# Optimization experiments

Hardware: AMD Instinct MI355X
Metric: run time of the kernel (lower is better)

The kernel has to match this reference:

```python
import jax, jax.numpy as jnp
import numpy as np
from jax import lax

Z_SIZE = 512
M = 512
HH = 511
BATCH = 65536


def setup_inputs() -> dict:
    key = jax.random.key(0)
    ks = jax.random.split(key, 5)
    z = jax.random.normal(ks[0], (BATCH, Z_SIZE), dtype=jnp.float32)
    # params initialized uniform(-1, 1) as in init_params
    v = jax.random.uniform(ks[1], (HH, Z_SIZE), dtype=jnp.float32, minval=-1.0, maxval=1.0)
    Rs = jax.random.uniform(ks[2], (M, M), dtype=jnp.float32, minval=-1.0, maxval=1.0)
    r2diag = jax.random.uniform(ks[3], (M,), dtype=jnp.float32, minval=-1.0, maxval=1.0)
    c = jax.random.uniform(ks[4], (1, M), dtype=jnp.float32, minval=-1.0, maxval=1.0)
    return {"z": z, "v": v, "Rs": Rs, "r2diag": r2diag, "c": c}


def _create_q(v):
    # normalize each Householder vector
    vn = v / jnp.linalg.norm(v, axis=1, keepdims=True)  # (hh, z)
    # q = prod_i (I - 2 v_i v_i^T), applied left-to-right.
    # Rank-1 update form: q <- q - 2 (q v_i) v_i^T  (O(n^2) per step).
    def body(q, vi):
        q = q - 2.0 * jnp.outer(q @ vi, vi)
        return q, None
    q, _ = lax.scan(body, jnp.eye(Z_SIZE, dtype=v.dtype), vn)
    return q[:, :M]  # (z_size, m)


def _create_rs(Rs, r2diag):
    r1 = jnp.triu(Rs, k=0)                     # (m, m)
    r2 = jnp.triu(Rs, k=1) + jnp.diag(r2diag)  # strict upper + learned diagonal
    return r1, r2


def reference(z, v, Rs, r2diag, c):
    r1, r2 = _create_rs(Rs, r2diag)
    q = _create_q(v)                 # (z, m)
    Bt = q @ r2.T                    # (z, m)
    A = q @ r1                       # (z, m)
    Btzc = z @ Bt + c                # (B, m)
    hB = jnp.tanh(Btzc)
    z_out = hB @ A.T + z             # (B, z)
    rrii = jnp.diagonal(r1) * jnp.diagonal(r2)  # (m,)
    der = 1.0 - hB * hB              # tanh'
    ldj = jnp.sum(jnp.log(jnp.abs(der * rrii + 1.0)), axis=1)  # (B,)
    return z_out, ldj
```

## Files before the change

kernel.cpp:

```cpp
#include <hip/hip_runtime.h>
#include <math.h>
#include <stdint.h>

#define ZDIM   512
#define MDIM   512
#define HHN    511
#define NBATCH 65536

typedef float f32x4 __attribute__((ext_vector_type(4)));
typedef short s16x8 __attribute__((ext_vector_type(8)));

__device__ __forceinline__ uint32_t bf16rne(float x) {
    uint32_t u = __float_as_uint(x);
    return (u + 0x7fffu + ((u >> 16) & 1u)) >> 16;
}
__device__ __forceinline__ void split2(float x, short& h, short& l) {
    uint32_t hu = bf16rne(x);
    float hf = __uint_as_float(hu << 16);
    uint32_t lu = bf16rne(x - hf);
    h = (short)hu; l = (short)lu;
}

__global__ void __launch_bounds__(64) prep_kernel(const float* __restrict__ v,
                                                  const float* __restrict__ Rs,
                                                  const float* __restrict__ r2diag,
                                                  float* __restrict__ vn,
                                                  float* __restrict__ rrii) {
    int b    = blockIdx.x;
    int lane = threadIdx.x;
    if (b < HHN) {
        const float4* src = reinterpret_cast<const float4*>(v + (size_t)b * ZDIM);
        float4 a0 = src[lane * 2];
        float4 a1 = src[lane * 2 + 1];
        float s = a0.x*a0.x + a0.y*a0.y + a0.z*a0.z + a0.w*a0.w
                + a1.x*a1.x + a1.y*a1.y + a1.z*a1.z + a1.w*a1.w;
#pragma unroll
        for (int off = 32; off >= 1; off >>= 1) s += __shfl_xor(s, off, 64);
        float inv = 1.0f / sqrtf(s);
        float4 o0 = make_float4(a0.x*inv, a0.y*inv, a0.z*inv, a0.w*inv);
        float4 o1 = make_float4(a1.x*inv, a1.y*inv, a1.z*inv, a1.w*inv);
        float4* dst = reinterpret_cast<float4*>(vn + (size_t)b * ZDIM);
        dst[lane * 2]     = o0;
        dst[lane * 2 + 1] = o1;
    } else {
        for (int m = lane; m < MDIM; m += 64)
            rrii[m] = Rs[(size_t)m * MDIM + m] * r2diag[m];
    }
}

__global__ void __launch_bounds__(256) householder_kernel(const float* __restrict__ vn,
                                                          float* __restrict__ Q) {
    int wave = threadIdx.x >> 6;
    int lane = threadIdx.x & 63;
    int r    = blockIdx.x * 4 + wave;

    float q[8];
#pragma unroll
    for (int j = 0; j < 8; ++j) q[j] = 0.0f;
    int base = r - lane * 8;
    if (base >= 0 && base < 8) q[base] = 1.0f;

    const float4* vn4 = reinterpret_cast<const float4*>(vn);
    float4 va = vn4[lane * 2];
    float4 vb = vn4[lane * 2 + 1];
    for (int i = 0; i < HHN; ++i) {
        float4 ca = va, cb = vb;
        if (i + 1 < HHN) {
            va = vn4[(size_t)(i + 1) * (ZDIM / 4) + lane * 2];
            vb = vn4[(size_t)(i + 1) * (ZDIM / 4) + lane * 2 + 1];
        }
        float d = q[0]*ca.x + q[1]*ca.y + q[2]*ca.z + q[3]*ca.w
                + q[4]*cb.x + q[5]*cb.y + q[6]*cb.z + q[7]*cb.w;
#pragma unroll
        for (int off = 32; off >= 1; off >>= 1) d += __shfl_xor(d, off, 64);
        float s = -2.0f * d;
        q[0] = fmaf(s, ca.x, q[0]); q[1] = fmaf(s, ca.y, q[1]);
        q[2] = fmaf(s, ca.z, q[2]); q[3] = fmaf(s, ca.w, q[3]);
        q[4] = fmaf(s, cb.x, q[4]); q[5] = fmaf(s, cb.y, q[5]);
        q[6] = fmaf(s, cb.z, q[6]); q[7] = fmaf(s, cb.w, q[7]);
    }
    float4* qdst = reinterpret_cast<float4*>(Q + (size_t)r * ZDIM);
    qdst[lane * 2]     = make_float4(q[0], q[1], q[2], q[3]);
    qdst[lane * 2 + 1] = make_float4(q[4], q[5], q[6], q[7]);
}

__global__ void __launch_bounds__(256) small_gemm_kernel(const float* __restrict__ Q,
                                                         const float* __restrict__ Rs,
                                                         const float* __restrict__ r2diag,
                                                         short* __restrict__ Ah_g,
                                                         short* __restrict__ Al_g,
                                                         short* __restrict__ B1h_g,
                                                         short* __restrict__ B1l_g) {
    int r0 = blockIdx.y * 64;
    int c0 = blockIdx.x * 64;
    int tid = threadIdx.x;
    int tx = tid & 15, ty = tid >> 4;

    __shared__ float Qs[16][68];
    __shared__ float RA[16][68];
    __shared__ float RB[16][68];

    float accA[4][4] = {};
    float accB[4][4] = {};

    for (int k0 = 0; k0 < ZDIM; k0 += 16) {
        {
            int r = tid >> 2, c4 = tid & 3;
            float4 g = *reinterpret_cast<const float4*>(Q + (size_t)(r0 + r) * ZDIM + k0 + c4 * 4);
            Qs[c4*4+0][r] = g.x; Qs[c4*4+1][r] = g.y; Qs[c4*4+2][r] = g.z; Qs[c4*4+3][r] = g.w;
        }
        {
            int kk = tid >> 4, c4 = tid & 15;
            int kg = k0 + kk, cg = c0 + c4 * 4;
            float4 g = *reinterpret_cast<const float4*>(Rs + (size_t)kg * MDIM + cg);
            float4 m;
            m.x = (kg <= cg + 0) ? g.x : 0.0f;
            m.y = (kg <= cg + 1) ? g.y : 0.0f;
            m.z = (kg <= cg + 2) ? g.z : 0.0f;
            m.w = (kg <= cg + 3) ? g.w : 0.0f;
            *reinterpret_cast<float4*>(&RA[kk][c4 * 4]) = m;
        }
        {
            int c = tid >> 2, k4 = tid & 3;
            int cg = c0 + c;
            float4 g = *reinterpret_cast<const float4*>(Rs + (size_t)cg * MDIM + k0 + k4 * 4);
            float gv[4] = {g.x, g.y, g.z, g.w};
#pragma unroll
            for (int qq = 0; qq < 4; ++qq) {
                int kg = k0 + k4 * 4 + qq;
                float val = (kg > cg) ? gv[qq] : ((kg == cg) ? r2diag[cg] : 0.0f);
                RB[k4 * 4 + qq][c] = val;
            }
        }
        __syncthreads();
#pragma unroll
        for (int kk = 0; kk < 16; ++kk) {
            float4 aq = *reinterpret_cast<const float4*>(&Qs[kk][ty * 4]);
            float4 ra = *reinterpret_cast<const float4*>(&RA[kk][tx * 4]);
            float4 rb = *reinterpret_cast<const float4*>(&RB[kk][tx * 4]);
            float av[4]  = {aq.x, aq.y, aq.z, aq.w};
            float rav[4] = {ra.x, ra.y, ra.z, ra.w};
            float rbv[4] = {rb.x, rb.y, rb.z, rb.w};
#pragma unroll
            for (int i = 0; i < 4; ++i)
#pragma unroll
                for (int j = 0; j < 4; ++j) {
                    accA[i][j] = fmaf(av[i], rav[j], accA[i][j]);
                    accB[i][j] = fmaf(av[i], rbv[j], accB[i][j]);
                }
        }
        __syncthreads();
    }
#pragma unroll
    for (int i = 0; i < 4; ++i) {
        int rg = r0 + ty * 4 + i;
#pragma unroll
        for (int j = 0; j < 4; ++j) {
            int cg = c0 + tx * 4 + j;
            short h, l;
            split2(accA[i][j], h, l);
            Ah_g[(size_t)rg * MDIM + cg] = h;
            Al_g[(size_t)rg * MDIM + cg] = l;
            split2(accB[i][j], h, l);
            B1h_g[(size_t)cg * ZDIM + rg] = h;
            B1l_g[(size_t)cg * ZDIM + rg] = l;
        }
    }
}

__global__ void __launch_bounds__(256, 2) gemm1_mfma(const float* __restrict__ z,
                                                     const short* __restrict__ B1h,
                                                     const short* __restrict__ B1l,
                                                     const float* __restrict__ cvec,
                                                     const float* __restrict__ rrii,
                                                     uint32_t* __restrict__ hBp,
                                                     float* __restrict__ ldj) {
    int b0 = blockIdx.x * 128;
    int c0 = blockIdx.y * 256;
    int tid = threadIdx.x;

    __shared__ short Azh[128][40], Azl[128][40];
    __shared__ short Bsh[256][40], Bsl[256][40];

    int wid = tid >> 6, lane = tid & 63;
    int wm = wid >> 1, wn = wid & 1;
    int lrow = lane & 15, lk = (lane >> 4) * 8;

    f32x4 acc[4][8];
#pragma unroll
    for (int m = 0; m < 4; ++m)
#pragma unroll
        for (int n = 0; n < 8; ++n) acc[m][n] = (f32x4){0.f, 0.f, 0.f, 0.f};

    for (int k0 = 0; k0 < ZDIM; k0 += 32) {
        {
            int r = tid >> 1, half = tid & 1;
            const float* zp = z + (size_t)(b0 + r) * ZDIM + k0 + half * 16;
            float xv[16];
            *reinterpret_cast<float4*>(&xv[0])  = *reinterpret_cast<const float4*>(zp);
            *reinterpret_cast<float4*>(&xv[4])  = *reinterpret_cast<const float4*>(zp + 4);
            *reinterpret_cast<float4*>(&xv[8])  = *reinterpret_cast<const float4*>(zp + 8);
            *reinterpret_cast<float4*>(&xv[12]) = *reinterpret_cast<const float4*>(zp + 12);
            s16x8 h0, h1, l0, l1;
#pragma unroll
            for (int j = 0; j < 8; ++j) { short hh, ll; split2(xv[j],     hh, ll); h0[j] = hh; l0[j] = ll; }
#pragma unroll
            for (int j = 0; j < 8; ++j) { short hh, ll; split2(xv[8 + j], hh, ll); h1[j] = hh; l1[j] = ll; }
            *reinterpret_cast<s16x8*>(&Azh[r][half * 16])     = h0;
            *reinterpret_cast<s16x8*>(&Azh[r][half * 16 + 8]) = h1;
            *reinterpret_cast<s16x8*>(&Azl[r][half * 16])     = l0;
            *reinterpret_cast<s16x8*>(&Azl[r][half * 16 + 8]) = l1;
        }
        {
            const short* ph = B1h + (size_t)(c0 + tid) * ZDIM + k0;
            const short* pl = B1l + (size_t)(c0 + tid) * ZDIM + k0;
#pragma unroll
            for (int s = 0; s < 4; ++s)
                *reinterpret_cast<s16x8*>(&Bsh[tid][s * 8]) = *reinterpret_cast<const s16x8*>(ph + s * 8);
#pragma unroll
            for (int s = 0; s < 4; ++s)
                *reinterpret_cast<s16x8*>(&Bsl[tid][s * 8]) = *reinterpret_cast<const s16x8*>(pl + s * 8);
        }
        __syncthreads();

        s16x8 ah[4], al[4];
#pragma unroll
        for (int m = 0; m < 4; ++m) {
            ah[m] = *reinterpret_cast<const s16x8*>(&Azh[wm * 64 + m * 16 + lrow][lk]);
            al[m] = *reinterpret_cast<const s16x8*>(&Azl[wm * 64 + m * 16 + lrow][lk]);
        }
#pragma unroll
        for (int n = 0; n < 8; ++n) {
            s16x8 bh = *reinterpret_cast<const s16x8*>(&Bsh[wn * 128 + n * 16 + lrow][lk]);
            s16x8 bl = *reinterpret_cast<const s16x8*>(&Bsl[wn * 128 + n * 16 + lrow][lk]);
#pragma unroll
            for (int m = 0; m < 4; ++m) {
                acc[m][n] = __builtin_amdgcn_mfma_f32_16x16x32_bf16(ah[m], bh, acc[m][n], 0, 0, 0);
                acc[m][n] = __builtin_amdgcn_mfma_f32_16x16x32_bf16(al[m], bh, acc[m][n], 0, 0, 0);
                acc[m][n] = __builtin_amdgcn_mfma_f32_16x16x32_bf16(ah[m], bl, acc[m][n], 0, 0, 0);
            }
        }
        __syncthreads();
    }

    float cv[8], rr[8];
#pragma unroll
    for (int n = 0; n < 8; ++n) {
        int col = c0 + wn * 128 + n * 16 + lrow;
        cv[n] = cvec[col];
        rr[n] = rrii[col];
    }
    float lsum[4][4];
#pragma unroll
    for (int m = 0; m < 4; ++m)
#pragma unroll
        for (int r = 0; r < 4; ++r) lsum[m][r] = 0.0f;

#pragma unroll
    for (int m = 0; m < 4; ++m) {
#pragma unroll
        for (int r = 0; r < 4; ++r) {
            int b = b0 + wm * 64 + m * 16 + (lane >> 4) * 4 + r;
#pragma unroll
            for (int n = 0; n < 8; ++n) {
                float val = acc[m][n][r] + cv[n];
                float h = tanhf(val);
                short hh, ll;
                split2(h, hh, ll);
                int col = c0 + wn * 128 + n * 16 + lrow;
                hBp[(size_t)b * MDIM + col] = (uint32_t)(uint16_t)hh | ((uint32_t)(uint16_t)ll << 16);
                float der = 1.0f - h * h;
                lsum[m][r] += logf(fabsf(fmaf(der, rr[n], 1.0f)));
            }
        }
    }
#pragma unroll
    for (int m = 0; m < 4; ++m) {
#pragma unroll
        for (int r = 0; r < 4; ++r) {
            float s = lsum[m][r];
            s += __shfl_xor(s, 1, 64);
            s += __shfl_xor(s, 2, 64);
            s += __shfl_xor(s, 4, 64);
            s += __shfl_xor(s, 8, 64);
            if ((lane & 15) == 0)
                atomicAdd(&ldj[b0 + wm * 64 + m * 16 + (lane >> 4) * 4 + r], s);
        }
    }
}

__global__ void __launch_bounds__(512, 2) gemm2_mfma(const float* __restrict__ z,
                                                     const short* __restrict__ Ah_g,
                                                     const short* __restrict__ Al_g,
                                                     float* __restrict__ out) {
    int b0 = blockIdx.x * 128;
    int tid = threadIdx.x;
    const uint32_t* hBp = reinterpret_cast<const uint32_t*>(out);

    __shared__ short Hh[128][40], Hl[128][40];
    __shared__ short Ash[512][40], Asl[512][40];

    int wid = tid >> 6, lane = tid & 63;
    int wm = wid >> 2, wn = wid & 3;
    int lrow = lane & 15, lk = (lane >> 4) * 8;

    f32x4 acc[4][8];
#pragma unroll
    for (int m = 0; m < 4; ++m)
#pragma unroll
        for (int n = 0; n < 8; ++n) acc[m][n] = (f32x4){0.f, 0.f, 0.f, 0.f};

    for (int m0 = 0; m0 < MDIM; m0 += 32) {
        {
            int r = tid >> 2, q = tid & 3;
            const uint32_t* hp = hBp + (size_t)(b0 + r) * MDIM + m0 + q * 8;
            uint4 u0 = *reinterpret_cast<const uint4*>(hp);
            uint4 u1 = *reinterpret_cast<const uint4*>(hp + 4);
            uint32_t uv[8] = {u0.x, u0.y, u0.z, u0.w, u1.x, u1.y, u1.z, u1.w};
            s16x8 vh, vl;
#pragma unroll
            for (int j = 0; j < 8; ++j) {
                vh[j] = (short)(uv[j] & 0xffffu);
                vl[j] = (short)(uv[j] >> 16);
            }
            *reinterpret_cast<s16x8*>(&Hh[r][q * 8]) = vh;
            *reinterpret_cast<s16x8*>(&Hl[r][q * 8]) = vl;
        }
        {
            const short* ph = Ah_g + (size_t)tid * MDIM + m0;
            const short* pl = Al_g + (size_t)tid * MDIM + m0;
#pragma unroll
            for (int s = 0; s < 4; ++s)
                *reinterpret_cast<s16x8*>(&Ash[tid][s * 8]) = *reinterpret_cast<const s16x8*>(ph + s * 8);
#pragma unroll
            for (int s = 0; s < 4; ++s)
                *reinterpret_cast<s16x8*>(&Asl[tid][s * 8]) = *reinterpret_cast<const s16x8*>(pl + s * 8);
        }
        __syncthreads();

        s16x8 ah[4], al[4];
#pragma unroll
        for (int m = 0; m < 4; ++m) {
            ah[m] = *reinterpret_cast<const s16x8*>(&Hh[wm * 64 + m * 16 + lrow][lk]);
            al[m] = *reinterpret_cast<const s16x8*>(&Hl[wm * 64 + m * 16 + lrow][lk]);
        }
#pragma unroll
        for (int n = 0; n < 8; ++n) {
            s16x8 bh = *reinterpret_cast<const s16x8*>(&Ash[wn * 128 + n * 16 + lrow][lk]);
            s16x8 bl = *reinterpret_cast<const s16x8*>(&Asl[wn * 128 + n * 16 + lrow][lk]);
#pragma unroll
            for (int m = 0; m < 4; ++m) {
                acc[m][n] = __builtin_amdgcn_mfma_f32_16x16x32_bf16(ah[m], bh, acc[m][n], 0, 0, 0);
                acc[m][n] = __builtin_amdgcn_mfma_f32_16x16x32_bf16(al[m], bh, acc[m][n], 0, 0, 0);
                acc[m][n] = __builtin_amdgcn_mfma_f32_16x16x32_bf16(ah[m], bl, acc[m][n], 0, 0, 0);
            }
        }
        __syncthreads();
    }

#pragma unroll
    for (int m = 0; m < 4; ++m) {
#pragma unroll
        for (int r = 0; r < 4; ++r) {
            int b = b0 + wm * 64 + m * 16 + (lane >> 4) * 4 + r;
#pragma unroll
            for (int n = 0; n < 8; ++n) {
                int colz = wn * 128 + n * 16 + lrow;
                out[(size_t)b * ZDIM + colz] = acc[m][n][r] + z[(size_t)b * ZDIM + colz];
            }
        }
    }
}

extern "C" void kernel_launch(void* const* d_in, const int* in_sizes, int n_in,
                              void* d_out, int out_size, void* d_ws, size_t ws_size,
                              hipStream_t stream) {
    const float* z      = (const float*)d_in[0];
    const float* v      = (const float*)d_in[1];
    const float* Rs     = (const float*)d_in[2];
    const float* r2diag = (const float*)d_in[3];
    const float* cvec   = (const float*)d_in[4];

    float* out = (float*)d_out;
    float* ldj = out + (size_t)NBATCH * ZDIM;

    float* ws   = (float*)d_ws;
    float* vn   = ws;
    float* Q    = ws + 262144;
    float* rrii = ws + 524288;
    short* sbase = (short*)(ws + 524800);
    short* Ah_g = sbase;
    short* Al_g = sbase + 262144;
    short* B1h  = sbase + 2 * 262144;
    short* B1l  = sbase + 3 * 262144;

    hipMemsetAsync(ldj, 0, NBATCH * sizeof(float), stream);

    prep_kernel<<<512, 64, 0, stream>>>(v, Rs, r2diag, vn, rrii);
    householder_kernel<<<128, 256, 0, stream>>>(vn, Q);
    small_gemm_kernel<<<dim3(8, 8), 256, 0, stream>>>(Q, Rs, r2diag, Ah_g, Al_g, B1h, B1l);
    gemm1_mfma<<<dim3(512, 2), 256, 0, stream>>>(z, B1h, B1l, cvec, rrii,
                                                 (uint32_t*)out, ldj);
    gemm2_mfma<<<512, 512, 0, stream>>>(z, Ah_g, Al_g, out);
}
```

Measured before the change: 718.9 us.

## Double-buffer activation tiles, read weight fragments from global, batch Householder rows per wave

Both MFMA GEMMs now keep only the activation tile in double-buffered shared memory, prefetching the next k-slice while computing, and read the small weight fragments directly from global (L2-resident) with a one-step register prefetch instead of staging them through LDS. gemm1 now uses 512 threads covering all 512 output columns per block, so z is split once per row block rather than twice. The Householder kernel has each wave process four rows of Q at once, sharing the vn loads and interleaving the four shuffle reductions, with a quarter of the blocks. The cost is more registers per thread and uncoalesced global weight reads that rely on cache hits.

```diff
diff --git a/kernel.cpp b/kernel.cpp
--- a/kernel.cpp
+++ b/kernel.cpp
@@ -50,15 +50,21 @@
 
 __global__ void __launch_bounds__(256) householder_kernel(const float* __restrict__ vn,
                                                           float* __restrict__ Q) {
-    int wave = threadIdx.x >> 6;
+    int wid  = threadIdx.x >> 6;
     int lane = threadIdx.x & 63;
-    int r    = blockIdx.x * 4 + wave;
-
-    float q[8];
-#pragma unroll
-    for (int j = 0; j < 8; ++j) q[j] = 0.0f;
-    int base = r - lane * 8;
-    if (base >= 0 && base < 8) q[base] = 1.0f;
+    int wslot = blockIdx.x * 4 + wid;
+
+    float q[4][8];
+#pragma unroll
+    for (int c = 0; c < 4; ++c)
+#pragma unroll
+        for (int j = 0; j < 8; ++j) q[c][j] = 0.0f;
+#pragma unroll
+    for (int c = 0; c < 4; ++c) {
+        int r = wslot * 4 + c;
+        int base = r - lane * 8;
+        if (base >= 0 && base < 8) q[c][base] = 1.0f;
+    }
 
     const float4* vn4 = reinterpret_cast<const float4*>(vn);
     float4 va = vn4[lane * 2];
@@ -69,19 +75,32 @@
             va = vn4[(size_t)(i + 1) * (ZDIM / 4) + lane * 2];
             vb = vn4[(size_t)(i + 1) * (ZDIM / 4) + lane * 2 + 1];
         }
-        float d = q[0]*ca.x + q[1]*ca.y + q[2]*ca.z + q[3]*ca.w
-                + q[4]*cb.x + q[5]*cb.y + q[6]*cb.z + q[7]*cb.w;
-#pragma unroll
-        for (int off = 32; off >= 1; off >>= 1) d += __shfl_xor(d, off, 64);
-        float s = -2.0f * d;
-        q[0] = fmaf(s, ca.x, q[0]); q[1] = fmaf(s, ca.y, q[1]);
-        q[2] = fmaf(s, ca.z, q[2]); q[3] = fmaf(s, ca.w, q[3]);
-        q[4] = fmaf(s, cb.x, q[4]); q[5] = fmaf(s, cb.y, q[5]);
-        q[6] = fmaf(s, cb.z, q[6]); q[7] = fmaf(s, cb.w, q[7]);
-    }
-    float4* qdst = reinterpret_cast<float4*>(Q + (size_t)r * ZDIM);
-    qdst[lane * 2]     = make_float4(q[0], q[1], q[2], q[3]);
-    qdst[lane * 2 + 1] = make_float4(q[4], q[5], q[6], q[7]);
+        float d[4];
+#pragma unroll
+        for (int c = 0; c < 4; ++c)
+            d[c] = q[c][0]*ca.x + q[c][1]*ca.y + q[c][2]*ca.z + q[c][3]*ca.w
+                 + q[c][4]*cb.x + q[c][5]*cb.y + q[c][6]*cb.z + q[c][7]*cb.w;
+#pragma unroll
+        for (int off = 32; off >= 1; off >>= 1) {
+#pragma unroll
+            for (int c = 0; c < 4; ++c) d[c] += __shfl_xor(d[c], off, 64);
+        }
+#pragma unroll
+        for (int c = 0; c < 4; ++c) {
+            float s = -2.0f * d[c];
+            q[c][0] = fmaf(s, ca.x, q[c][0]); q[c][1] = fmaf(s, ca.y, q[c][1]);
+            q[c][2] = fmaf(s, ca.z, q[c][2]); q[c][3] = fmaf(s, ca.w, q[c][3]);
+            q[c][4] = fmaf(s, cb.x, q[c][4]); q[c][5] = fmaf(s, cb.y, q[c][5]);
+            q[c][6] = fmaf(s, cb.z, q[c][6]); q[c][7] = fmaf(s, cb.w, q[c][7]);
+        }
+    }
+#pragma unroll
+    for (int c = 0; c < 4; ++c) {
+        int r = wslot * 4 + c;
+        float4* qdst = reinterpret_cast<float4*>(Q + (size_t)r * ZDIM);
+        qdst[lane * 2]     = make_float4(q[c][0], q[c][1], q[c][2], q[c][3]);
+        qdst[lane * 2 + 1] = make_float4(q[c][4], q[c][5], q[c][6], q[c][7]);
+    }
 }
 
 __global__ void __launch_bounds__(256) small_gemm_kernel(const float* __restrict__ Q,
@@ -168,7 +187,7 @@
     }
 }
 
-__global__ void __launch_bounds__(256, 2) gemm1_mfma(const float* __restrict__ z,
+__global__ void __launch_bounds__(512, 2) gemm1_mfma(const float* __restrict__ z,
                                                      const short* __restrict__ B1h,
                                                      const short* __restrict__ B1l,
                                                      const float* __restrict__ cvec,
@@ -176,15 +195,14 @@
                                                      uint32_t* __restrict__ hBp,
                                                      float* __restrict__ ldj) {
     int b0 = blockIdx.x * 128;
-    int c0 = blockIdx.y * 256;
     int tid = threadIdx.x;
 
-    __shared__ short Azh[128][40], Azl[128][40];
-    __shared__ short Bsh[256][40], Bsl[256][40];
+    __shared__ short Azh[2][128][40], Azl[2][128][40];
 
     int wid = tid >> 6, lane = tid & 63;
-    int wm = wid >> 1, wn = wid & 1;
+    int wm = wid >> 2, wn = wid & 3;
     int lrow = lane & 15, lk = (lane >> 4) * 8;
+    int srow = tid >> 2, squar = tid & 3;
 
     f32x4 acc[4][8];
 #pragma unroll
@@ -192,53 +210,61 @@
 #pragma unroll
         for (int n = 0; n < 8; ++n) acc[m][n] = (f32x4){0.f, 0.f, 0.f, 0.f};
 
-    for (int k0 = 0; k0 < ZDIM; k0 += 32) {
-        {
-            int r = tid >> 1, half = tid & 1;
-            const float* zp = z + (size_t)(b0 + r) * ZDIM + k0 + half * 16;
-            float xv[16];
-            *reinterpret_cast<float4*>(&xv[0])  = *reinterpret_cast<const float4*>(zp);
-            *reinterpret_cast<float4*>(&xv[4])  = *reinterpret_cast<const float4*>(zp + 4);
-            *reinterpret_cast<float4*>(&xv[8])  = *reinterpret_cast<const float4*>(zp + 8);
-            *reinterpret_cast<float4*>(&xv[12]) = *reinterpret_cast<const float4*>(zp + 12);
-            s16x8 h0, h1, l0, l1;
-#pragma unroll
-            for (int j = 0; j < 8; ++j) { short hh, ll; split2(xv[j],     hh, ll); h0[j] = hh; l0[j] = ll; }
-#pragma unroll
-            for (int j = 0; j < 8; ++j) { short hh, ll; split2(xv[8 + j], hh, ll); h1[j] = hh; l1[j] = ll; }
-            *reinterpret_cast<s16x8*>(&Azh[r][half * 16])     = h0;
-            *reinterpret_cast<s16x8*>(&Azh[r][half * 16 + 8]) = h1;
-            *reinterpret_cast<s16x8*>(&Azl[r][half * 16])     = l0;
-            *reinterpret_cast<s16x8*>(&Azl[r][half * 16 + 8]) = l1;
-        }
-        {
-            const short* ph = B1h + (size_t)(c0 + tid) * ZDIM + k0;
-            const short* pl = B1l + (size_t)(c0 + tid) * ZDIM + k0;
-#pragma unroll
-            for (int s = 0; s < 4; ++s)
-                *reinterpret_cast<s16x8*>(&Bsh[tid][s * 8]) = *reinterpret_cast<const s16x8*>(ph + s * 8);
-#pragma unroll
-            for (int s = 0; s < 4; ++s)
-                *reinterpret_cast<s16x8*>(&Bsl[tid][s * 8]) = *reinterpret_cast<const s16x8*>(pl + s * 8);
-        }
-        __syncthreads();
-
+    float4 za, zb;
+    const float* zrow = z + (size_t)(b0 + srow) * ZDIM + squar * 8;
+    const short* bhbase = B1h + (size_t)(wn * 128 + lrow) * ZDIM + lk;
+    const short* blbase = B1l + (size_t)(wn * 128 + lrow) * ZDIM + lk;
+
+    za = *reinterpret_cast<const float4*>(zrow);
+    zb = *reinterpret_cast<const float4*>(zrow + 4);
+    {
+        s16x8 h, l;
+#pragma unroll
+        for (int j = 0; j < 4; ++j) { short hh, ll; split2((&za.x)[j], hh, ll); h[j] = hh; l[j] = ll; }
+#pragma unroll
+        for (int j = 0; j < 4; ++j) { short hh, ll; split2((&zb.x)[j], hh, ll); h[4+j] = hh; l[4+j] = ll; }
+        *reinterpret_cast<s16x8*>(&Azh[0][srow][squar * 8]) = h;
+        *reinterpret_cast<s16x8*>(&Azl[0][srow][squar * 8]) = l;
+    }
+    __syncthreads();
+
+    for (int t = 0; t < 16; ++t) {
+        int k0 = t * 32, cur = t & 1;
+        if (t + 1 < 16) {
+            za = *reinterpret_cast<const float4*>(zrow + (t + 1) * 32);
+            zb = *reinterpret_cast<const float4*>(zrow + (t + 1) * 32 + 4);
+        }
         s16x8 ah[4], al[4];
 #pragma unroll
         for (int m = 0; m < 4; ++m) {
-            ah[m] = *reinterpret_cast<const s16x8*>(&Azh[wm * 64 + m * 16 + lrow][lk]);
-            al[m] = *reinterpret_cast<const s16x8*>(&Azl[wm * 64 + m * 16 + lrow][lk]);
-        }
+            ah[m] = *reinterpret_cast<const s16x8*>(&Azh[cur][wm * 64 + m * 16 + lrow][lk]);
+            al[m] = *reinterpret_cast<const s16x8*>(&Azl[cur][wm * 64 + m * 16 + lrow][lk]);
+        }
+        s16x8 bh = *reinterpret_cast<const s16x8*>(bhbase + k0);
+        s16x8 bl = *reinterpret_cast<const s16x8*>(blbase + k0);
 #pragma unroll
         for (int n = 0; n < 8; ++n) {
-            s16x8 bh = *reinterpret_cast<const s16x8*>(&Bsh[wn * 128 + n * 16 + lrow][lk]);
-            s16x8 bl = *reinterpret_cast<const s16x8*>(&Bsl[wn * 128 + n * 16 + lrow][lk]);
+            s16x8 nbh, nbl;
+            if (n < 7) {
+                nbh = *reinterpret_cast<const s16x8*>(bhbase + (size_t)(n + 1) * 16 * ZDIM + k0);
+                nbl = *reinterpret_cast<const s16x8*>(blbase + (size_t)(n + 1) * 16 * ZDIM + k0);
+            }
 #pragma unroll
             for (int m = 0; m < 4; ++m) {
                 acc[m][n] = __builtin_amdgcn_mfma_f32_16x16x32_bf16(ah[m], bh, acc[m][n], 0, 0, 0);
                 acc[m][n] = __builtin_amdgcn_mfma_f32_16x16x32_bf16(al[m], bh, acc[m][n], 0, 0, 0);
                 acc[m][n] = __builtin_amdgcn_mfma_f32_16x16x32_bf16(ah[m], bl, acc[m][n], 0, 0, 0);
             }
+            bh = nbh; bl = nbl;
+        }
+        if (t + 1 < 16) {
+            s16x8 h, l;
+#pragma unroll
+            for (int j = 0; j < 4; ++j) { short hh, ll; split2((&za.x)[j], hh, ll); h[j] = hh; l[j] = ll; }
+#pragma unroll
+            for (int j = 0; j < 4; ++j) { short hh, ll; split2((&zb.x)[j], hh, ll); h[4+j] = hh; l[4+j] = ll; }
+            *reinterpret_cast<s16x8*>(&Azh[cur ^ 1][srow][squar * 8]) = h;
+            *reinterpret_cast<s16x8*>(&Azl[cur ^ 1][srow][squar * 8]) = l;
         }
         __syncthreads();
     }
@@ -246,7 +272,7 @@
     float cv[8], rr[8];
 #pragma unroll
     for (int n = 0; n < 8; ++n) {
-        int col = c0 + wn * 128 + n * 16 + lrow;
+        int col = wn * 128 + n * 16 + lrow;
         cv[n] = cvec[col];
         rr[n] = rrii[col];
     }
@@ -267,7 +293,7 @@
                 float h = tanhf(val);
                 short hh, ll;
                 split2(h, hh, ll);
-                int col = c0 + wn * 128 + n * 16 + lrow;
+                int col = wn * 128 + n * 16 + lrow;
                 hBp[(size_t)b * MDIM + col] = (uint32_t)(uint16_t)hh | ((uint32_t)(uint16_t)ll << 16);
                 float der = 1.0f - h * h;
                 lsum[m][r] += logf(fabsf(fmaf(der, rr[n], 1.0f)));
@@ -297,12 +323,12 @@
     int tid = threadIdx.x;
     const uint32_t* hBp = reinterpret_cast<const uint32_t*>(out);
 
-    __shared__ short Hh[128][40], Hl[128][40];
-    __shared__ short Ash[512][40], Asl[512][40];
+    __shared__ short Hh[2][128][40], Hl[2][128][40];
 
     int wid = tid >> 6, lane = tid & 63;
     int wm = wid >> 2, wn = wid & 3;
     int lrow = lane & 15, lk = (lane >> 4) * 8;
+    int srow = tid >> 2, squar = tid & 3;
 
     f32x4 acc[4][8];
 #pragma unroll
@@ -310,50 +336,59 @@
 #pragma unroll
         for (int n = 0; n < 8; ++n) acc[m][n] = (f32x4){0.f, 0.f, 0.f, 0.f};
 
-    for (int m0 = 0; m0 < MDIM; m0 += 32) {
-        {
-            int r = tid >> 2, q = tid & 3;
-            const uint32_t* hp = hBp + (size_t)(b0 + r) * MDIM + m0 + q * 8;
-            uint4 u0 = *reinterpret_cast<const uint4*>(hp);
-            uint4 u1 = *reinterpret_cast<const uint4*>(hp + 4);
-            uint32_t uv[8] = {u0.x, u0.y, u0.z, u0.w, u1.x, u1.y, u1.z, u1.w};
-            s16x8 vh, vl;
-#pragma unroll
-            for (int j = 0; j < 8; ++j) {
-                vh[j] = (short)(uv[j] & 0xffffu);
-                vl[j] = (short)(uv[j] >> 16);
-            }
-            *reinterpret_cast<s16x8*>(&Hh[r][q * 8]) = vh;
-            *reinterpret_cast<s16x8*>(&Hl[r][q * 8]) = vl;
-        }
-        {
-            const short* ph = Ah_g + (size_t)tid * MDIM + m0;
-            const short* pl = Al_g + (size_t)tid * MDIM + m0;
-#pragma unroll
-            for (int s = 0; s < 4; ++s)
-                *reinterpret_cast<s16x8*>(&Ash[tid][s * 8]) = *reinterpret_cast<const s16x8*>(ph + s * 8);
-#pragma unroll
-            for (int s = 0; s < 4; ++s)
-                *reinterpret_cast<s16x8*>(&Asl[tid][s * 8]) = *reinterpret_cast<const s16x8*>(pl + s * 8);
-        }
-        __syncthreads();
-
+    uint4 ua, ub;
+    const uint32_t* hrow = hBp + (size_t)(b0 + srow) * MDIM + squar * 8;
+    const short* bhbase = Ah_g + (size_t)(wn * 128 + lrow) * MDIM + lk;
+    const short* blbase = Al_g + (size_t)(wn * 128 + lrow) * MDIM + lk;
+
+    ua = *reinterpret_cast<const uint4*>(hrow);
+    ub = *reinterpret_cast<const uint4*>(hrow + 4);
+    {
+        s16x8 h, l;
+        uint32_t uv[8] = {ua.x, ua.y, ua.z, ua.w, ub.x, ub.y, ub.z, ub.w};
+#pragma unroll
+        for (int j = 0; j < 8; ++j) { h[j] = (short)(uv[j] & 0xffffu); l[j] = (short)(uv[j] >> 16); }
+        *reinterpret_cast<s16x8*>(&Hh[0][srow][squar * 8]) = h;
+        *reinterpret_cast<s16x8*>(&Hl[0][srow][squar * 8]) = l;
+    }
+    __syncthreads();
+
+    for (int t = 0; t < 16; ++t) {
+        int m0 = t * 32, cur = t & 1;
+        if (t + 1 < 16) {
+            ua = *reinterpret_cast<const uint4*>(hrow + (t + 1) * 32);
+            ub = *reinterpret_cast<const uint4*>(hrow + (t + 1) * 32 + 4);
+        }
         s16x8 ah[4], al[4];
 #pragma unroll
         for (int m = 0; m < 4; ++m) {
-            ah[m] = *reinterpret_cast<const s16x8*>(&Hh[wm * 64 + m * 16 + lrow][lk]);
-            al[m] = *reinterpret_cast<const s16x8*>(&Hl[wm * 64 + m * 16 + lrow][lk]);
-        }
+            ah[m] = *reinterpret_cast<const s16x8*>(&Hh[cur][wm * 64 + m * 16 + lrow][lk]);
+            al[m] = *reinterpret_cast<const s16x8*>(&Hl[cur][wm * 64 + m * 16 + lrow][lk]);
+        }
+        s16x8 bh = *reinterpret_cast<const s16x8*>(bhbase + m0);
+        s16x8 bl = *reinterpret_cast<const s16x8*>(blbase + m0);
 #pragma unroll
         for (int n = 0; n < 8; ++n) {
-            s16x8 bh = *reinterpret_cast<const s16x8*>(&Ash[wn * 128 + n * 16 + lrow][lk]);
-            s16x8 bl = *reinterpret_cast<const s16x8*>(&Asl[wn * 128 + n * 16 + lrow][lk]);
+            s16x8 nbh, nbl;
+            if (n < 7) {
+                nbh = *reinterpret_cast<const s16x8*>(bhbase + (size_t)(n + 1) * 16 * MDIM + m0);
+                nbl = *reinterpret_cast<const s16x8*>(blbase + (size_t)(n + 1) * 16 * MDIM + m0);
+            }
 #pragma unroll
             for (int m = 0; m < 4; ++m) {
                 acc[m][n] = __builtin_amdgcn_mfma_f32_16x16x32_bf16(ah[m], bh, acc[m][n], 0, 0, 0);
                 acc[m][n] = __builtin_amdgcn_mfma_f32_16x16x32_bf16(al[m], bh, acc[m][n], 0, 0, 0);
                 acc[m][n] = __builtin_amdgcn_mfma_f32_16x16x32_bf16(ah[m], bl, acc[m][n], 0, 0, 0);
             }
+            bh = nbh; bl = nbl;
+        }
+        if (t + 1 < 16) {
+            s16x8 h, l;
+            uint32_t uv[8] = {ua.x, ua.y, ua.z, ua.w, ub.x, ub.y, ub.z, ub.w};
+#pragma unroll
+            for (int j = 0; j < 8; ++j) { h[j] = (short)(uv[j] & 0xffffu); l[j] = (short)(uv[j] >> 16); }
+            *reinterpret_cast<s16x8*>(&Hh[cur ^ 1][srow][squar * 8]) = h;
+            *reinterpret_cast<s16x8*>(&Hl[cur ^ 1][srow][squar * 8]) = l;
         }
         __syncthreads();
     }
@@ -397,9 +432,8 @@
     hipMemsetAsync(ldj, 0, NBATCH * sizeof(float), stream);
 
     prep_kernel<<<512, 64, 0, stream>>>(v, Rs, r2diag, vn, rrii);
-    householder_kernel<<<128, 256, 0, stream>>>(vn, Q);
+    householder_kernel<<<32, 256, 0, stream>>>(vn, Q);
     small_gemm_kernel<<<dim3(8, 8), 256, 0, stream>>>(Q, Rs, r2diag, Ah_g, Al_g, B1h, B1l);
-    gemm1_mfma<<<dim3(512, 2), 256, 0, stream>>>(z, B1h, B1l, cvec, rrii,
-                                                 (uint32_t*)out, ldj);
+    gemm1_mfma<<<512, 512, 0, stream>>>(z, B1h, B1l, cvec, rrii, (uint32_t*)out, ldj);
     gemm2_mfma<<<512, 512, 0, stream>>>(z, Ah_g, Al_g, out);
 }
```

Measured after the change: 984.0 us. +36.9%, slower.

## Replace sequential Householder product with blocked compact-WY formulation

Applied to the files above, without the earlier changes.

Builds Q via a Gram matrix of normalized Householder vectors, a blocked triangular recurrence (partial GEMM plus in-block trisolve per 64-column panel), and a final GEMM forming I - 2·D·V. This removes the 511-step serial loop with wave-wide shuffle reductions in the old kernel. In exchange it adds roughly 17 extra kernel launches, including single-block trisolves, more total FLOPs, and a possible change in rounding behaviour.

```diff
diff --git a/kernel.cpp b/kernel.cpp
--- a/kernel.cpp
+++ b/kernel.cpp
@@ -45,43 +45,195 @@
     } else {
         for (int m = lane; m < MDIM; m += 64)
             rrii[m] = Rs[(size_t)m * MDIM + m] * r2diag[m];
-    }
-}
-
-__global__ void __launch_bounds__(256) householder_kernel(const float* __restrict__ vn,
-                                                          float* __restrict__ Q) {
-    int wave = threadIdx.x >> 6;
-    int lane = threadIdx.x & 63;
-    int r    = blockIdx.x * 4 + wave;
-
-    float q[8];
-#pragma unroll
-    for (int j = 0; j < 8; ++j) q[j] = 0.0f;
-    int base = r - lane * 8;
-    if (base >= 0 && base < 8) q[base] = 1.0f;
-
-    const float4* vn4 = reinterpret_cast<const float4*>(vn);
-    float4 va = vn4[lane * 2];
-    float4 vb = vn4[lane * 2 + 1];
-    for (int i = 0; i < HHN; ++i) {
-        float4 ca = va, cb = vb;
-        if (i + 1 < HHN) {
-            va = vn4[(size_t)(i + 1) * (ZDIM / 4) + lane * 2];
-            vb = vn4[(size_t)(i + 1) * (ZDIM / 4) + lane * 2 + 1];
-        }
-        float d = q[0]*ca.x + q[1]*ca.y + q[2]*ca.z + q[3]*ca.w
-                + q[4]*cb.x + q[5]*cb.y + q[6]*cb.z + q[7]*cb.w;
-#pragma unroll
-        for (int off = 32; off >= 1; off >>= 1) d += __shfl_xor(d, off, 64);
-        float s = -2.0f * d;
-        q[0] = fmaf(s, ca.x, q[0]); q[1] = fmaf(s, ca.y, q[1]);
-        q[2] = fmaf(s, ca.z, q[2]); q[3] = fmaf(s, ca.w, q[3]);
-        q[4] = fmaf(s, cb.x, q[4]); q[5] = fmaf(s, cb.y, q[5]);
-        q[6] = fmaf(s, cb.z, q[6]); q[7] = fmaf(s, cb.w, q[7]);
-    }
-    float4* qdst = reinterpret_cast<float4*>(Q + (size_t)r * ZDIM);
-    qdst[lane * 2]     = make_float4(q[0], q[1], q[2], q[3]);
-    qdst[lane * 2 + 1] = make_float4(q[4], q[5], q[6], q[7]);
+        float4 z4 = make_float4(0.f, 0.f, 0.f, 0.f);
+        float4* dst = reinterpret_cast<float4*>(vn + (size_t)HHN * ZDIM);
+        dst[lane * 2]     = z4;
+        dst[lane * 2 + 1] = z4;
+    }
+}
+
+__global__ void __launch_bounds__(256) gram_kernel(const float* __restrict__ vn,
+                                                   float* __restrict__ G) {
+    int i0 = blockIdx.y * 64;
+    int j0 = blockIdx.x * 64;
+    int tid = threadIdx.x;
+    int tx = tid & 15, ty = tid >> 4;
+
+    __shared__ float Ai[16][68];
+    __shared__ float Bj[16][68];
+
+    float acc[4][4] = {};
+    for (int k0 = 0; k0 < ZDIM; k0 += 16) {
+        {
+            int r = tid >> 2, c4 = tid & 3;
+            float4 g = *reinterpret_cast<const float4*>(vn + (size_t)(i0 + r) * ZDIM + k0 + c4 * 4);
+            Ai[c4*4+0][r] = g.x; Ai[c4*4+1][r] = g.y; Ai[c4*4+2][r] = g.z; Ai[c4*4+3][r] = g.w;
+        }
+        {
+            int r = tid >> 2, c4 = tid & 3;
+            float4 g = *reinterpret_cast<const float4*>(vn + (size_t)(j0 + r) * ZDIM + k0 + c4 * 4);
+            Bj[c4*4+0][r] = g.x; Bj[c4*4+1][r] = g.y; Bj[c4*4+2][r] = g.z; Bj[c4*4+3][r] = g.w;
+        }
+        __syncthreads();
+#pragma unroll
+        for (int kk = 0; kk < 16; ++kk) {
+            float4 a4 = *reinterpret_cast<const float4*>(&Ai[kk][ty * 4]);
+            float4 b4 = *reinterpret_cast<const float4*>(&Bj[kk][tx * 4]);
+            float av[4] = {a4.x, a4.y, a4.z, a4.w};
+            float bv[4] = {b4.x, b4.y, b4.z, b4.w};
+#pragma unroll
+            for (int i = 0; i < 4; ++i)
+#pragma unroll
+                for (int j = 0; j < 4; ++j)
+                    acc[i][j] = fmaf(av[i], bv[j], acc[i][j]);
+        }
+        __syncthreads();
+    }
+#pragma unroll
+    for (int i = 0; i < 4; ++i)
+#pragma unroll
+        for (int j = 0; j < 4; ++j)
+            G[(size_t)(i0 + ty * 4 + i) * ZDIM + j0 + tx * 4 + j] = acc[i][j];
+}
+
+__global__ void __launch_bounds__(256) partial_kernel(float* __restrict__ D,
+                                                      const float* __restrict__ G,
+                                                      const float* __restrict__ vn,
+                                                      int b) {
+    int r0 = blockIdx.x * 64;
+    int c0 = b * 64;
+    int K  = c0;
+    int tid = threadIdx.x;
+    int tx = tid & 15, ty = tid >> 4;
+
+    __shared__ float As[16][68];
+    __shared__ float Bs[16][68];
+
+    float acc[4][4] = {};
+    for (int k0 = 0; k0 < K; k0 += 16) {
+        {
+            int r = tid >> 2, c4 = tid & 3;
+            float4 g = *reinterpret_cast<const float4*>(D + (size_t)(r0 + r) * ZDIM + k0 + c4 * 4);
+            As[c4*4+0][r] = g.x; As[c4*4+1][r] = g.y; As[c4*4+2][r] = g.z; As[c4*4+3][r] = g.w;
+        }
+        {
+            int kk = tid >> 4, c4 = tid & 15;
+            float4 g = *reinterpret_cast<const float4*>(G + (size_t)(k0 + kk) * ZDIM + c0 + c4 * 4);
+            *reinterpret_cast<float4*>(&Bs[kk][c4 * 4]) = g;
+        }
+        __syncthreads();
+#pragma unroll
+        for (int kk = 0; kk < 16; ++kk) {
+            float4 a4 = *reinterpret_cast<const float4*>(&As[kk][ty * 4]);
+            float4 b4 = *reinterpret_cast<const float4*>(&Bs[kk][tx * 4]);
+            float av[4] = {a4.x, a4.y, a4.z, a4.w};
+            float bv[4] = {b4.x, b4.y, b4.z, b4.w};
+#pragma unroll
+            for (int i = 0; i < 4; ++i)
+#pragma unroll
+                for (int j = 0; j < 4; ++j)
+                    acc[i][j] = fmaf(av[i], bv[j], acc[i][j]);
+        }
+        __syncthreads();
+    }
+#pragma unroll
+    for (int i = 0; i < 4; ++i) {
+        int rg = r0 + ty * 4 + i;
+#pragma unroll
+        for (int j = 0; j < 4; ++j) {
+            int cg = c0 + tx * 4 + j;
+            D[(size_t)rg * ZDIM + cg] = vn[(size_t)cg * ZDIM + rg] - 2.0f * acc[i][j];
+        }
+    }
+}
+
+__global__ void __launch_bounds__(512) trisolve_kernel(float* __restrict__ D,
+                                                       const float* __restrict__ G,
+                                                       int b) {
+    __shared__ float Gs[64][65];
+    int tid = threadIdx.x;
+    int c0 = b * 64;
+    {
+        int i = tid >> 3, j8 = (tid & 7) * 8;
+        const float* gp = G + (size_t)(c0 + i) * ZDIM + c0 + j8;
+        float4 g0 = *reinterpret_cast<const float4*>(gp);
+        float4 g1 = *reinterpret_cast<const float4*>(gp + 4);
+        Gs[i][j8+0] = -2.0f*g0.x; Gs[i][j8+1] = -2.0f*g0.y;
+        Gs[i][j8+2] = -2.0f*g0.z; Gs[i][j8+3] = -2.0f*g0.w;
+        Gs[i][j8+4] = -2.0f*g1.x; Gs[i][j8+5] = -2.0f*g1.y;
+        Gs[i][j8+6] = -2.0f*g1.z; Gs[i][j8+7] = -2.0f*g1.w;
+    }
+    __syncthreads();
+
+    float dl[64];
+    float* drow = D + (size_t)tid * ZDIM + c0;
+#pragma unroll
+    for (int q = 0; q < 16; ++q) {
+        float4 t = *reinterpret_cast<const float4*>(drow + q * 4);
+        dl[q*4+0] = t.x; dl[q*4+1] = t.y; dl[q*4+2] = t.z; dl[q*4+3] = t.w;
+    }
+#pragma unroll
+    for (int j = 0; j < 64; ++j) {
+        float acc = dl[j];
+#pragma unroll
+        for (int i = 0; i < j; ++i)
+            acc = fmaf(dl[i], Gs[i][j], acc);
+        dl[j] = acc;
+    }
+#pragma unroll
+    for (int q = 0; q < 16; ++q) {
+        float4 t = make_float4(dl[q*4+0], dl[q*4+1], dl[q*4+2], dl[q*4+3]);
+        *reinterpret_cast<float4*>(drow + q * 4) = t;
+    }
+}
+
+__global__ void __launch_bounds__(256) qbuild_kernel(const float* __restrict__ D,
+                                                     const float* __restrict__ vn,
+                                                     float* __restrict__ Q) {
+    int r0 = blockIdx.y * 64;
+    int c0 = blockIdx.x * 64;
+    int tid = threadIdx.x;
+    int tx = tid & 15, ty = tid >> 4;
+
+    __shared__ float As[16][68];
+    __shared__ float Bs[16][68];
+
+    float acc[4][4] = {};
+    for (int k0 = 0; k0 < ZDIM; k0 += 16) {
+        {
+            int r = tid >> 2, c4 = tid & 3;
+            float4 g = *reinterpret_cast<const float4*>(D + (size_t)(r0 + r) * ZDIM + k0 + c4 * 4);
+            As[c4*4+0][r] = g.x; As[c4*4+1][r] = g.y; As[c4*4+2][r] = g.z; As[c4*4+3][r] = g.w;
+        }
+        {
+            int kk = tid >> 4, c4 = tid & 15;
+            float4 g = *reinterpret_cast<const float4*>(vn + (size_t)(k0 + kk) * ZDIM + c0 + c4 * 4);
+            *reinterpret_cast<float4*>(&Bs[kk][c4 * 4]) = g;
+        }
+        __syncthreads();
+#pragma unroll
+        for (int kk = 0; kk < 16; ++kk) {
+            float4 a4 = *reinterpret_cast<const float4*>(&As[kk][ty * 4]);
+            float4 b4 = *reinterpret_cast<const float4*>(&Bs[kk][tx * 4]);
+            float av[4] = {a4.x, a4.y, a4.z, a4.w};
+            float bv[4] = {b4.x, b4.y, b4.z, b4.w};
+#pragma unroll
+            for (int i = 0; i < 4; ++i)
+#pragma unroll
+                for (int j = 0; j < 4; ++j)
+                    acc[i][j] = fmaf(av[i], bv[j], acc[i][j]);
+        }
+        __syncthreads();
+    }
+#pragma unroll
+    for (int i = 0; i < 4; ++i) {
+        int rg = r0 + ty * 4 + i;
+#pragma unroll
+        for (int j = 0; j < 4; ++j) {
+            int cg = c0 + tx * 4 + j;
+            Q[(size_t)rg * ZDIM + cg] = (rg == cg ? 1.0f : 0.0f) - 2.0f * acc[i][j];
+        }
+    }
 }
 
 __global__ void __launch_bounds__(256) small_gemm_kernel(const float* __restrict__ Q,
@@ -387,8 +539,10 @@
     float* ws   = (float*)d_ws;
     float* vn   = ws;
     float* Q    = ws + 262144;
-    float* rrii = ws + 524288;
-    short* sbase = (short*)(ws + 524800);
+    float* G    = ws + 2 * 262144;
+    float* D    = ws + 3 * 262144;
+    float* rrii = ws + 4 * 262144;
+    short* sbase = (short*)(ws + 4 * 262144 + 512);
     short* Ah_g = sbase;
     short* Al_g = sbase + 262144;
     short* B1h  = sbase + 2 * 262144;
@@ -397,9 +551,13 @@
     hipMemsetAsync(ldj, 0, NBATCH * sizeof(float), stream);
 
     prep_kernel<<<512, 64, 0, stream>>>(v, Rs, r2diag, vn, rrii);
-    householder_kernel<<<128, 256, 0, stream>>>(vn, Q);
+    gram_kernel<<<dim3(8, 8), 256, 0, stream>>>(vn, G);
+    for (int b = 0; b < 8; ++b) {
+        partial_kernel<<<8, 256, 0, stream>>>(D, G, vn, b);
+        trisolve_kernel<<<1, 512, 0, stream>>>(D, G, b);
+    }
+    qbuild_kernel<<<dim3(8, 8), 256, 0, stream>>>(D, vn, Q);
     small_gemm_kernel<<<dim3(8, 8), 256, 0, stream>>>(Q, Rs, r2diag, Ah_g, Al_g, B1h, B1l);
-    gemm1_mfma<<<dim3(512, 2), 256, 0, stream>>>(z, B1h, B1l, cvec, rrii,
-                                                 (uint32_t*)out, ldj);
+    gemm1_mfma<<<dim3(512, 2), 256, 0, stream>>>(z, B1h, B1l, cvec, rrii, (uint32_t*)out, ldj);
     gemm2_mfma<<<512, 512, 0, stream>>>(z, Ah_g, Al_g, out);
 }
```

After: 1.047 ms. +45.6%, slower.
